# Performance work log

Measured on AMD Instinct MI355X. Metric: run time of the kernel, lower is better.

Reference implementation:

```python
import jax, jax.numpy as jnp
import numpy as np

DIM_Q = 1024
DIM_K = 1024
DIM_V = 1024


def setup_inputs() -> dict:
    key = jax.random.key(0)
    kx, kq, kk, kv = jax.random.split(key, 4)
    x = jax.random.normal(kx, (4, 2048, DIM_Q), dtype=jnp.float32)
    # torch nn.Linear weights: [out_features, in_features], y = x @ W.T
    scale = 1.0 / np.sqrt(DIM_Q)
    Wq = jax.random.uniform(kq, (DIM_K, DIM_Q), dtype=jnp.float32, minval=-scale, maxval=scale)
    Wk = jax.random.uniform(kk, (DIM_K, DIM_Q), dtype=jnp.float32, minval=-scale, maxval=scale)
    Wv = jax.random.uniform(kv, (DIM_V, DIM_Q), dtype=jnp.float32, minval=-scale, maxval=scale)
    return {"x": x, "Wq": Wq, "Wk": Wk, "Wv": Wv}


def reference(x, Wq, Wk, Wv):
    # q, k: [b, s, dim_k]; v: [b, s, dim_v]
    q = jnp.einsum('bsd,kd->bsk', x, Wq)
    k = jnp.einsum('bsd,kd->bsk', x, Wk)
    v = jnp.einsum('bsd,vd->bsv', x, Wv)
    norm_fact = 1.0 / jnp.sqrt(jnp.asarray(DIM_K, dtype=x.dtype))
    score = jnp.einsum('bik,bjk->bij', q, k) * norm_fact  # [b, s, s]
    score = jax.nn.softmax(score, axis=-1)
    att = jnp.einsum('bij,bjv->biv', score, v)
    att = att + v  # is_residual=True
    return att
```

## Files before the change

kernel.cpp:

```cpp
#include <hip/hip_runtime.h>
#include <hip/hip_bf16.h>

using bf16 = __hip_bfloat16;
typedef __attribute__((ext_vector_type(8))) short short8;
typedef __attribute__((ext_vector_type(4))) float floatx4;
typedef __attribute__((ext_vector_type(8))) int int8v;

__device__ __forceinline__ void async_ld16(const void* g, void* l) {
  __builtin_amdgcn_global_load_lds((const __attribute__((address_space(1))) void*)g,
                                   (__attribute__((address_space(3))) void*)l, 16, 0, 0);
}

__device__ __forceinline__ int pk4_fp8(float a, float b, float c, float d) {
  int v = __builtin_amdgcn_cvt_pk_fp8_f32(a, b, 0, false);
  return __builtin_amdgcn_cvt_pk_fp8_f32(c, d, v, true);
}

__device__ __forceinline__ int8v ld_frag16(const unsigned char* lo, const unsigned char* hi) {
  int4 l0 = *(const int4*)lo, h0 = *(const int4*)hi;
  int8v v;
  v[0] = l0.x; v[1] = l0.y; v[2] = l0.z; v[3] = l0.w;
  v[4] = h0.x; v[5] = h0.y; v[6] = h0.z; v[7] = h0.w;
  return v;
}


__device__ __forceinline__ void gemm_core(const bf16* __restrict__ At,
                                          const bf16* __restrict__ Bt,
                                          int K, bf16* lA, bf16* lB,
                                          floatx4 acc[4][4]) {
  const int tid  = threadIdx.x;
  const int w    = tid >> 6;
  const int lane = tid & 63;
  const int subM = (w >> 1) * 64;
  const int subN = (w & 1) * 64;
  const int fr   = lane & 15;
  const int fq   = lane >> 4;

  int srow[4], scol[4], sdst[4];
#pragma unroll
  for (int q = 0; q < 4; ++q) {
    int p = q * 256 + w * 64 + lane;
    int r = p >> 3;
    int j = (p & 7) ^ (r & 7);
    srow[q] = r;
    scol[q] = j * 8;
    sdst[q] = (q * 256 + w * 64) * 8;
  }
  int offA[2][4], offB[2][4];
#pragma unroll
  for (int kc = 0; kc < 2; ++kc)
#pragma unroll
    for (int i = 0; i < 4; ++i) {
      int rA = subM + i * 16 + fr;
      offA[kc][i] = (rA * 8 + ((kc * 4 + fq) ^ (rA & 7))) * 8;
      int rB = subN + i * 16 + fr;
      offB[kc][i] = (rB * 8 + ((kc * 4 + fq) ^ (rB & 7))) * 8;
    }

  floatx4 zero = {0.f, 0.f, 0.f, 0.f};
#pragma unroll
  for (int i = 0; i < 4; ++i)
#pragma unroll
    for (int j = 0; j < 4; ++j) acc[i][j] = zero;

  for (int k0 = 0; k0 < K; k0 += 64) {
    __syncthreads();
#pragma unroll
    for (int q = 0; q < 4; ++q) {
      async_ld16(At + (size_t)srow[q] * K + k0 + scol[q], lA + sdst[q]);
      async_ld16(Bt + (size_t)srow[q] * K + k0 + scol[q], lB + sdst[q]);
    }
    __syncthreads();
#pragma unroll
    for (int kc = 0; kc < 2; ++kc) {
      short8 a[4], b[4];
#pragma unroll
      for (int i = 0; i < 4; ++i) a[i] = *(const short8*)(lA + offA[kc][i]);
#pragma unroll
      for (int j = 0; j < 4; ++j) b[j] = *(const short8*)(lB + offB[kc][j]);
#pragma unroll
      for (int i = 0; i < 4; ++i)
#pragma unroll
        for (int j = 0; j < 4; ++j)
          acc[i][j] = __builtin_amdgcn_mfma_f32_16x16x32_bf16(a[i], b[j], acc[i][j], 0, 0, 0);
    }
  }
}

__device__ __forceinline__ void gemm_core_f8(const unsigned char* __restrict__ At,
                                             const unsigned char* __restrict__ Bt,
                                             int K, unsigned char* lA, unsigned char* lB,
                                             floatx4 acc[4][4]) {
  const int tid  = threadIdx.x;
  const int w    = tid >> 6;
  const int lane = tid & 63;
  const int subM = (w >> 1) * 64;
  const int subN = (w & 1) * 64;
  const int fr   = lane & 15;
  const int fq   = lane >> 4;

  int srow[4], scol[4], sdst[4];
#pragma unroll
  for (int q = 0; q < 4; ++q) {
    int p = q * 256 + w * 64 + lane;
    int r = p >> 3;
    int j = (p & 7) ^ (r & 7) ^ ((r & 8) >> 1);
    srow[q] = r;
    scol[q] = j * 16;
    sdst[q] = (q * 256 + w * 64) * 16;
  }
  int offA[2][4], offB[2][4];
#pragma unroll
  for (int h = 0; h < 2; ++h)
#pragma unroll
    for (int i = 0; i < 4; ++i) {
      int rA = subM + i * 16 + fr;
      offA[h][i] = rA * 128 + (((fq * 2 + h) ^ (rA & 7) ^ ((rA & 8) >> 1)) * 16);
      int rB = subN + i * 16 + fr;
      offB[h][i] = rB * 128 + (((fq * 2 + h) ^ (rB & 7) ^ ((rB & 8) >> 1)) * 16);
    }

  floatx4 zero = {0.f, 0.f, 0.f, 0.f};
#pragma unroll
  for (int i = 0; i < 4; ++i)
#pragma unroll
    for (int j = 0; j < 4; ++j) acc[i][j] = zero;

  for (int k0 = 0; k0 < K; k0 += 128) {
    __syncthreads();
#pragma unroll
    for (int q = 0; q < 4; ++q) {
      async_ld16(At + (size_t)srow[q] * K + k0 + scol[q], lA + sdst[q]);
      async_ld16(Bt + (size_t)srow[q] * K + k0 + scol[q], lB + sdst[q]);
    }
    __syncthreads();
    int8v a[4], b[4];
#pragma unroll
    for (int i = 0; i < 4; ++i) a[i] = ld_frag16(lA + offA[0][i], lA + offA[1][i]);
#pragma unroll
    for (int j = 0; j < 4; ++j) b[j] = ld_frag16(lB + offB[0][j], lB + offB[1][j]);
#pragma unroll
    for (int i = 0; i < 4; ++i)
#pragma unroll
      for (int j = 0; j < 4; ++j)
        acc[i][j] = __builtin_amdgcn_mfma_scale_f32_16x16x128_f8f6f4(
            a[i], b[j], acc[i][j], 0, 0, 0, 0x7F7F7F7F, 0, 0x7F7F7F7F);
  }
}

__device__ __forceinline__ void gemm_core_f8_v2(const unsigned char* __restrict__ At,
                                                const unsigned char* __restrict__ Bt,
                                                int K, unsigned char* lA, unsigned char* lB,
                                                floatx4 acc[4][8]) {
  const int tid  = threadIdx.x;
  const int w    = tid >> 6;
  const int lane = tid & 63;
  const int subM = (w >> 1) * 64;
  const int subN = (w & 1) * 128;
  const int fr   = lane & 15;
  const int fq   = lane >> 4;

  int srowA[4], scolA[4], sdstA[4];
#pragma unroll
  for (int q = 0; q < 4; ++q) {
    int p = q * 256 + w * 64 + lane;
    int r = p >> 3;
    int j = (p & 7) ^ (r & 7) ^ ((r & 8) >> 1);
    srowA[q] = r; scolA[q] = j * 16; sdstA[q] = (q * 256 + w * 64) * 16;
  }
  int srowB[8], scolB[8], sdstB[8];
#pragma unroll
  for (int q = 0; q < 8; ++q) {
    int p = q * 256 + w * 64 + lane;
    int r = p >> 3;
    int j = (p & 7) ^ (r & 7) ^ ((r & 8) >> 1);
    srowB[q] = r; scolB[q] = j * 16; sdstB[q] = (q * 256 + w * 64) * 16;
  }
  int offA[2][4], offB[2][8];
#pragma unroll
  for (int h = 0; h < 2; ++h) {
#pragma unroll
    for (int i = 0; i < 4; ++i) {
      int rA = subM + i * 16 + fr;
      offA[h][i] = rA * 128 + (((fq * 2 + h) ^ (rA & 7) ^ ((rA & 8) >> 1)) * 16);
    }
#pragma unroll
    for (int j = 0; j < 8; ++j) {
      int rB = subN + j * 16 + fr;
      offB[h][j] = rB * 128 + (((fq * 2 + h) ^ (rB & 7) ^ ((rB & 8) >> 1)) * 16);
    }
  }

  floatx4 zero = {0.f, 0.f, 0.f, 0.f};
#pragma unroll
  for (int i = 0; i < 4; ++i)
#pragma unroll
    for (int j = 0; j < 8; ++j) acc[i][j] = zero;

  for (int k0 = 0; k0 < K; k0 += 128) {
    __syncthreads();
#pragma unroll
    for (int q = 0; q < 4; ++q)
      async_ld16(At + (size_t)srowA[q] * K + k0 + scolA[q], lA + sdstA[q]);
#pragma unroll
    for (int q = 0; q < 8; ++q)
      async_ld16(Bt + (size_t)srowB[q] * K + k0 + scolB[q], lB + sdstB[q]);
    __syncthreads();
    int8v a[4];
#pragma unroll
    for (int i = 0; i < 4; ++i) a[i] = ld_frag16(lA + offA[0][i], lA + offA[1][i]);
#pragma unroll
    for (int j = 0; j < 8; ++j) {
      int8v bf = ld_frag16(lB + offB[0][j], lB + offB[1][j]);
#pragma unroll
      for (int i = 0; i < 4; ++i)
        acc[i][j] = __builtin_amdgcn_mfma_scale_f32_16x16x128_f8f6f4(
            a[i], bf, acc[i][j], 0, 0, 0, 0x7F7F7F7F, 0, 0x7F7F7F7F);
    }
  }
}

__global__ __launch_bounds__(256, 2) void proj_gemm(
    const bf16* __restrict__ Xbf, const bf16* __restrict__ Wvbf, bf16* __restrict__ Vbf,
    const unsigned char* __restrict__ X8, const unsigned char* __restrict__ Wq8,
    const unsigned char* __restrict__ Wk8,
    unsigned char* __restrict__ Qf8, unsigned char* __restrict__ Kf8) {
  __shared__ __align__(16) char lds[49152];
  const int id = blockIdx.x;
  const int tid = threadIdx.x, w = tid >> 6, lane = tid & 63;
  const int fr = lane & 15, fq = lane >> 4;

  if (id < 512) {
    const int r = id & 7, g = id >> 3;
    const int ty = r * 8 + (g & 7), tx = g >> 3;
    bf16* lA = (bf16*)lds;
    bf16* lB = (bf16*)(lds + 16384);
    floatx4 acc[4][4];
    gemm_core(Xbf + (size_t)ty * 128 * 1024, Wvbf + (size_t)tx * 128 * 1024,
              1024, lA, lB, acc);
    const int subM = (w >> 1) * 64, subN = (w & 1) * 64;
    const int rowBase = ty * 128 + subM;
    const int colBase = tx * 128 + subN;
#pragma unroll
    for (int i = 0; i < 4; ++i)
#pragma unroll
      for (int j = 0; j < 4; ++j)
#pragma unroll
        for (int rr = 0; rr < 4; ++rr) {
          int row = rowBase + i * 16 + fq * 4 + rr;
          int col = colBase + j * 16 + fr;
          Vbf[(size_t)row * 1024 + col] = __float2bfloat16(acc[i][j][rr]);
        }
  } else {
    const int local = id - 512;
    const int z = local >> 8, lid = local & 255;
    const int r = lid & 7, g = lid >> 3;
    const int ty = r * 8 + (g & 7);
    const int tx = g >> 3;
    unsigned char* lA = (unsigned char*)lds;
    unsigned char* lB = (unsigned char*)(lds + 16384);
    floatx4 acc[4][8];
    gemm_core_f8_v2(X8 + (size_t)ty * 128 * 1024,
                    (z == 0 ? Wq8 : Wk8) + (size_t)tx * 256 * 1024, 1024, lA, lB, acc);
    unsigned char* dst = (z == 0) ? Qf8 : Kf8;
    const int subM = (w >> 1) * 64, subN = (w & 1) * 128;
    const int rowBase = ty * 128 + subM;
    const int colBase = tx * 256 + subN;
#pragma unroll
    for (int i = 0; i < 4; ++i)
#pragma unroll
      for (int rr = 0; rr < 4; ++rr) {
        int row = rowBase + i * 16 + fq * 4 + rr;
        unsigned int p0 = (unsigned int)pk4_fp8(acc[i][0][rr], acc[i][1][rr],
                                                acc[i][2][rr], acc[i][3][rr]);
        unsigned int p1 = (unsigned int)pk4_fp8(acc[i][4][rr], acc[i][5][rr],
                                                acc[i][6][rr], acc[i][7][rr]);
        *(unsigned int*)&dst[(size_t)row * 1024 + colBase + fr * 4] = p0;
        *(unsigned int*)&dst[(size_t)row * 1024 + colBase + 64 + fr * 4] = p1;
      }
  }
}

__global__ __launch_bounds__(256, 2) void mid_kernel(
    const unsigned char* __restrict__ Qf8, const unsigned char* __restrict__ Kf8,
    unsigned char* __restrict__ S8, float* __restrict__ l,
    const bf16* __restrict__ Vbf, unsigned char* __restrict__ Vt8) {
  __shared__ __align__(16) char lds[49152];
  const int id = blockIdx.x;
  const int t = threadIdx.x;

  if (id < 512) {
    const int r = id & 7, g = id >> 3;
    const int b = g >> 4;
    const int rem = g & 15;
    const int ty = r * 2 + (rem & 1);
    const int tx = rem >> 1;
    unsigned char* lA = (unsigned char*)lds;
    unsigned char* lB = (unsigned char*)(lds + 16384);
    floatx4 acc[4][8];
    gemm_core_f8_v2(Qf8 + (size_t)b * 2048 * 1024 + (size_t)ty * 128 * 1024,
                    Kf8 + (size_t)b * 2048 * 1024 + (size_t)tx * 256 * 1024,
                    1024, lA, lB, acc);
    const int w = t >> 6, lane = t & 63;
    const int subM = (w >> 1) * 64, subN = (w & 1) * 128;
    const int fr = lane & 15, fq = lane >> 4;
    const int rowBase = ty * 128 + subM;
    const int colBase = tx * 256 + subN;
    unsigned char* Sb = S8 + (size_t)b * 2048 * 2048;
    float* lb = l + (size_t)b * 2048;
#pragma unroll
    for (int i = 0; i < 4; ++i)
#pragma unroll
      for (int rr = 0; rr < 4; ++rr) {
        int row = rowBase + i * 16 + fq * 4 + rr;
        unsigned int p0 = (unsigned int)pk4_fp8(
            __expf(acc[i][0][rr] * 0.03125f), __expf(acc[i][1][rr] * 0.03125f),
            __expf(acc[i][2][rr] * 0.03125f), __expf(acc[i][3][rr] * 0.03125f));
        unsigned int p1 = (unsigned int)pk4_fp8(
            __expf(acc[i][4][rr] * 0.03125f), __expf(acc[i][5][rr] * 0.03125f),
            __expf(acc[i][6][rr] * 0.03125f), __expf(acc[i][7][rr] * 0.03125f));
        *(unsigned int*)&Sb[(size_t)row * 2048 + colBase + fr * 4] = p0;
        *(unsigned int*)&Sb[(size_t)row * 2048 + colBase + 64 + fr * 4] = p1;
        float psum = __builtin_amdgcn_cvt_f32_fp8(p0, 0) + __builtin_amdgcn_cvt_f32_fp8(p0, 1) +
                     __builtin_amdgcn_cvt_f32_fp8(p0, 2) + __builtin_amdgcn_cvt_f32_fp8(p0, 3) +
                     __builtin_amdgcn_cvt_f32_fp8(p1, 0) + __builtin_amdgcn_cvt_f32_fp8(p1, 1) +
                     __builtin_amdgcn_cvt_f32_fp8(p1, 2) + __builtin_amdgcn_cvt_f32_fp8(p1, 3);
        psum += __shfl_xor(psum, 1, 64);
        psum += __shfl_xor(psum, 2, 64);
        psum += __shfl_xor(psum, 4, 64);
        psum += __shfl_xor(psum, 8, 64);
        if (fr == 0) atomicAdd(&lb[row], psum);
      }
  } else {
    const int t2 = id - 512;
    const int b = t2 >> 9, rem = t2 & 511;
    const int xs = rem & 31, yv = rem >> 5;
    const int s0 = xs * 64, v0 = yv * 64;
    short(*tile)[72] = (short(*)[72])lds;
#pragma unroll
    for (int i = 0; i < 2; ++i) {
      int c = t + i * 256;
      int row = c >> 3, cj = c & 7;
      *(short8*)&tile[row][cj * 8] =
          *(const short8*)&Vbf[((size_t)(b * 2048 + s0 + row)) * 1024 + v0 + cj * 8];
    }
    __syncthreads();
    const int vrow = t >> 2, sq = t & 3;
#pragma unroll
    for (int hc = 0; hc < 2; ++hc) {
      float f[8];
#pragma unroll
      for (int e = 0; e < 8; ++e) {
        int p = sq * 16 + hc * 8 + e;
        int s = (p & 3) * 16 + (p >> 2);
        short sh = tile[s][vrow];
        f[e] = __bfloat162float(*(bf16*)&sh);
      }
      uint2 packed;
      packed.x = (unsigned int)pk4_fp8(f[0], f[1], f[2], f[3]);
      packed.y = (unsigned int)pk4_fp8(f[4], f[5], f[6], f[7]);
      *(uint2*)&Vt8[((size_t)(b * 1024 + v0 + vrow)) * 2048 + s0 + sq * 16 + hc * 8] = packed;
    }
  }
}

__global__ __launch_bounds__(256) void pv_gemm(const unsigned char* __restrict__ S8,
                                               const unsigned char* __restrict__ Vt8,
                                               const bf16* __restrict__ Vbf,
                                               const float* __restrict__ l,
                                               float* __restrict__ out) {
  __shared__ __align__(16) char lds[32768];
  unsigned char* lA = (unsigned char*)lds;
  unsigned char* lB = (unsigned char*)(lds + 16384);
  const int id = blockIdx.x;
  const int r = id & 7, g = id >> 3;
  const int b = g >> 4;
  const int rem = g & 15;
  const int ty = r * 2 + (rem & 1);
  const int tx = rem >> 1;

  floatx4 acc[4][4];
  gemm_core_f8(S8 + (size_t)b * 2048 * 2048 + (size_t)ty * 128 * 2048,
               Vt8 + (size_t)b * 1024 * 2048 + (size_t)tx * 128 * 2048,
               2048, lA, lB, acc);

  const int tid = threadIdx.x, w = tid >> 6, lane = tid & 63;
  const int subM = (w >> 1) * 64, subN = (w & 1) * 64;
  const int fr = lane & 15, fq = lane >> 4;
  const int rowBase = ty * 128 + subM;
  const int colBase = tx * 128 + subN;
  const float* lb = l + (size_t)b * 2048;
#pragma unroll
  for (int i = 0; i < 4; ++i)
#pragma unroll
    for (int rr = 0; rr < 4; ++rr) {
      int row = rowBase + i * 16 + fq * 4 + rr;
      float inv = 1.0f / lb[row];
#pragma unroll
      for (int j = 0; j < 4; ++j) {
        int col = colBase + j * 16 + fr;
        size_t oi = ((size_t)b * 2048 + row) * 1024 + col;
        out[oi] = acc[i][j][rr] * inv + __bfloat162float(Vbf[oi]);
      }
    }
}

__global__ void cast_all(const float* __restrict__ x, const float* __restrict__ wq,
                         const float* __restrict__ wk, const float* __restrict__ wv,
                         bf16* __restrict__ Xbf, unsigned char* __restrict__ X8,
                         unsigned char* __restrict__ Wq8, unsigned char* __restrict__ Wk8,
                         bf16* __restrict__ Wvbf, float* __restrict__ l) {
  const int blk = blockIdx.x;
  const int t = threadIdx.x;
  if (blk < 2048) {
#pragma unroll
    for (int k = 0; k < 4; ++k) {
      int i = blk * 1024 + k * 256 + t;
      float4 f = ((const float4*)x)[i];
      bf16 tmp[4] = {__float2bfloat16(f.x), __float2bfloat16(f.y),
                     __float2bfloat16(f.z), __float2bfloat16(f.w)};
      ((ushort4*)Xbf)[i] = *(const ushort4*)tmp;
      ((unsigned int*)X8)[i] = (unsigned int)pk4_fp8(f.x, f.y, f.z, f.w);
    }
  } else if (blk < 2560) {
    const float* src = (blk < 2304) ? wq : wk;
    unsigned char* dst = (blk < 2304) ? Wq8 : Wk8;
    int base = ((blk - 2048) & 255) * 1024;
#pragma unroll
    for (int k = 0; k < 4; ++k) {
      int i = base + k * 256 + t;
      float4 f = ((const float4*)src)[i];
      ((unsigned int*)dst)[i] = (unsigned int)pk4_fp8(f.x, f.y, f.z, f.w);
    }
  } else if (blk < 2816) {
#pragma unroll
    for (int k = 0; k < 4; ++k) {
      int i = (blk - 2560) * 1024 + k * 256 + t;
      float4 f = ((const float4*)wv)[i];
      bf16 tmp[4] = {__float2bfloat16(f.x), __float2bfloat16(f.y),
                     __float2bfloat16(f.z), __float2bfloat16(f.w)};
      ((ushort4*)Wvbf)[i] = *(const ushort4*)tmp;
    }
  } else {
#pragma unroll
    for (int k = 0; k < 8; ++k)
      ((float4*)l)[k * 256 + t] = make_float4(0.f, 0.f, 0.f, 0.f);
  }
}

extern "C" void kernel_launch(void* const* d_in, const int* in_sizes, int n_in,
                              void* d_out, int out_size, void* d_ws, size_t ws_size,
                              hipStream_t stream) {
  const float* x  = (const float*)d_in[0];
  const float* Wq = (const float*)d_in[1];
  const float* Wk = (const float*)d_in[2];
  const float* Wv = (const float*)d_in[3];
  float* out = (float*)d_out;

  char* ws = (char*)d_ws;
  bf16* Xbf = (bf16*)ws;                   ws += (size_t)8192 * 1024 * 2;
  unsigned char* X8 = (unsigned char*)ws;  ws += (size_t)8192 * 1024;
  unsigned char* Wq8 = (unsigned char*)ws; ws += (size_t)1024 * 1024;
  unsigned char* Wk8 = (unsigned char*)ws; ws += (size_t)1024 * 1024;
  bf16* Wvbf = (bf16*)ws;                  ws += (size_t)1024 * 1024 * 2;
  unsigned char* Qf8 = (unsigned char*)ws; ws += (size_t)8192 * 1024;
  unsigned char* Kf8 = (unsigned char*)ws; ws += (size_t)8192 * 1024;
  bf16* Vbf = (bf16*)ws;                   ws += (size_t)8192 * 1024 * 2;
  unsigned char* Vt8 = (unsigned char*)ws; ws += (size_t)4 * 1024 * 2048;
  unsigned char* S8  = (unsigned char*)ws; ws += (size_t)4 * 2048 * 2048;
  float* l = (float*)ws;                   ws += (size_t)8192 * 4;

  cast_all<<<2817, 256, 0, stream>>>(x, Wq, Wk, Wv, Xbf, X8, Wq8, Wk8, Wvbf, l);
  proj_gemm<<<1024, 256, 0, stream>>>(Xbf, Wvbf, Vbf, X8, Wq8, Wk8, Qf8, Kf8);
  mid_kernel<<<2560, 256, 0, stream>>>(Qf8, Kf8, S8, l, Vbf, Vt8);
  pv_gemm<<<512, 256, 0, stream>>>(S8, Vt8, Vbf, l, out);
}
```

Before: 176.3 us.

## Double-buffer PV GEMM with 128x256 tiles and async prefetch pipeline

Rewrites the PV GEMM to use 128x256 output tiles, halving the grid to 256 blocks. It also adds a double-buffered LDS pipeline, so the next K-tile is prefetched with global_load_lds while MFMAs run on the current one, using explicit vmcnt waits and s_setprio. This is meant to hide global-load latency and raise reuse of each S tile, at the cost of 96KB LDS per block, which limits occupancy. With only 256 blocks on a 256-CU device, there is a single wave of work and little latency hiding across blocks. The final iteration issues a redundant prefetch of tile 0.

Measured after the change: 180.9 us. +2.6%, slower.

```diff
diff --git a/kernel.cpp b/kernel.cpp
--- a/kernel.cpp
+++ b/kernel.cpp
@@ -88,67 +88,6 @@
   }
 }
 
-__device__ __forceinline__ void gemm_core_f8(const unsigned char* __restrict__ At,
-                                             const unsigned char* __restrict__ Bt,
-                                             int K, unsigned char* lA, unsigned char* lB,
-                                             floatx4 acc[4][4]) {
-  const int tid  = threadIdx.x;
-  const int w    = tid >> 6;
-  const int lane = tid & 63;
-  const int subM = (w >> 1) * 64;
-  const int subN = (w & 1) * 64;
-  const int fr   = lane & 15;
-  const int fq   = lane >> 4;
-
-  int srow[4], scol[4], sdst[4];
-#pragma unroll
-  for (int q = 0; q < 4; ++q) {
-    int p = q * 256 + w * 64 + lane;
-    int r = p >> 3;
-    int j = (p & 7) ^ (r & 7) ^ ((r & 8) >> 1);
-    srow[q] = r;
-    scol[q] = j * 16;
-    sdst[q] = (q * 256 + w * 64) * 16;
-  }
-  int offA[2][4], offB[2][4];
-#pragma unroll
-  for (int h = 0; h < 2; ++h)
-#pragma unroll
-    for (int i = 0; i < 4; ++i) {
-      int rA = subM + i * 16 + fr;
-      offA[h][i] = rA * 128 + (((fq * 2 + h) ^ (rA & 7) ^ ((rA & 8) >> 1)) * 16);
-      int rB = subN + i * 16 + fr;
-      offB[h][i] = rB * 128 + (((fq * 2 + h) ^ (rB & 7) ^ ((rB & 8) >> 1)) * 16);
-    }
-
-  floatx4 zero = {0.f, 0.f, 0.f, 0.f};
-#pragma unroll
-  for (int i = 0; i < 4; ++i)
-#pragma unroll
-    for (int j = 0; j < 4; ++j) acc[i][j] = zero;
-
-  for (int k0 = 0; k0 < K; k0 += 128) {
-    __syncthreads();
-#pragma unroll
-    for (int q = 0; q < 4; ++q) {
-      async_ld16(At + (size_t)srow[q] * K + k0 + scol[q], lA + sdst[q]);
-      async_ld16(Bt + (size_t)srow[q] * K + k0 + scol[q], lB + sdst[q]);
-    }
-    __syncthreads();
-    int8v a[4], b[4];
-#pragma unroll
-    for (int i = 0; i < 4; ++i) a[i] = ld_frag16(lA + offA[0][i], lA + offA[1][i]);
-#pragma unroll
-    for (int j = 0; j < 4; ++j) b[j] = ld_frag16(lB + offB[0][j], lB + offB[1][j]);
-#pragma unroll
-    for (int i = 0; i < 4; ++i)
-#pragma unroll
-      for (int j = 0; j < 4; ++j)
-        acc[i][j] = __builtin_amdgcn_mfma_scale_f32_16x16x128_f8f6f4(
-            a[i], b[j], acc[i][j], 0, 0, 0, 0x7F7F7F7F, 0, 0x7F7F7F7F);
-  }
-}
-
 __device__ __forceinline__ void gemm_core_f8_v2(const unsigned char* __restrict__ At,
                                                 const unsigned char* __restrict__ Bt,
                                                 int K, unsigned char* lA, unsigned char* lB,
@@ -218,6 +157,97 @@
         acc[i][j] = __builtin_amdgcn_mfma_scale_f32_16x16x128_f8f6f4(
             a[i], bf, acc[i][j], 0, 0, 0, 0x7F7F7F7F, 0, 0x7F7F7F7F);
     }
+  }
+}
+
+__device__ __forceinline__ void gemm_core_f8_v2_dbuf(const unsigned char* __restrict__ At,
+                                                     const unsigned char* __restrict__ Bt,
+                                                     int K, unsigned char* lds0,
+                                                     floatx4 acc[4][8]) {
+  const int tid  = threadIdx.x;
+  const int w    = tid >> 6;
+  const int lane = tid & 63;
+  const int subM = (w >> 1) * 64;
+  const int subN = (w & 1) * 128;
+  const int fr   = lane & 15;
+  const int fq   = lane >> 4;
+
+  int srowA[4], scolA[4], sdstA[4];
+#pragma unroll
+  for (int q = 0; q < 4; ++q) {
+    int p = q * 256 + w * 64 + lane;
+    int r = p >> 3;
+    int j = (p & 7) ^ (r & 7) ^ ((r & 8) >> 1);
+    srowA[q] = r; scolA[q] = j * 16; sdstA[q] = (q * 256 + w * 64) * 16;
+  }
+  int srowB[8], scolB[8], sdstB[8];
+#pragma unroll
+  for (int q = 0; q < 8; ++q) {
+    int p = q * 256 + w * 64 + lane;
+    int r = p >> 3;
+    int j = (p & 7) ^ (r & 7) ^ ((r & 8) >> 1);
+    srowB[q] = r; scolB[q] = j * 16; sdstB[q] = (q * 256 + w * 64) * 16;
+  }
+  int offA[2][4], offB[2][8];
+#pragma unroll
+  for (int h = 0; h < 2; ++h) {
+#pragma unroll
+    for (int i = 0; i < 4; ++i) {
+      int rA = subM + i * 16 + fr;
+      offA[h][i] = rA * 128 + (((fq * 2 + h) ^ (rA & 7) ^ ((rA & 8) >> 1)) * 16);
+    }
+#pragma unroll
+    for (int j = 0; j < 8; ++j) {
+      int rB = subN + j * 16 + fr;
+      offB[h][j] = rB * 128 + (((fq * 2 + h) ^ (rB & 7) ^ ((rB & 8) >> 1)) * 16);
+    }
+  }
+
+  auto stage = [&](int buf, int k0) {
+    unsigned char* base = lds0 + buf * 49152;
+#pragma unroll
+    for (int q = 0; q < 4; ++q)
+      async_ld16(At + (size_t)srowA[q] * K + k0 + scolA[q], base + sdstA[q]);
+#pragma unroll
+    for (int q = 0; q < 8; ++q)
+      async_ld16(Bt + (size_t)srowB[q] * K + k0 + scolB[q], base + 16384 + sdstB[q]);
+  };
+
+  floatx4 zero = {0.f, 0.f, 0.f, 0.f};
+#pragma unroll
+  for (int i = 0; i < 4; ++i)
+#pragma unroll
+    for (int j = 0; j < 8; ++j) acc[i][j] = zero;
+
+  const int nt = K >> 7;
+  stage(0, 0);
+  asm volatile("s_waitcnt vmcnt(0)" ::: "memory");
+  __builtin_amdgcn_s_barrier();
+
+  for (int t = 0; t < nt; ++t) {
+    const int nb = (t + 1) & 1;
+    const int tn = (t + 1 < nt) ? (t + 1) : 0;
+    stage(nb, tn << 7);
+    asm volatile("s_waitcnt vmcnt(12)" ::: "memory");
+    __builtin_amdgcn_s_barrier();
+    __builtin_amdgcn_sched_barrier(0);
+
+    const unsigned char* lA = lds0 + (t & 1) * 49152;
+    const unsigned char* lB = lA + 16384;
+    int8v a[4];
+#pragma unroll
+    for (int i = 0; i < 4; ++i) a[i] = ld_frag16(lA + offA[0][i], lA + offA[1][i]);
+    __builtin_amdgcn_s_setprio(1);
+#pragma unroll
+    for (int j = 0; j < 8; ++j) {
+      int8v bf = ld_frag16(lB + offB[0][j], lB + offB[1][j]);
+#pragma unroll
+      for (int i = 0; i < 4; ++i)
+        acc[i][j] = __builtin_amdgcn_mfma_scale_f32_16x16x128_f8f6f4(
+            a[i], bf, acc[i][j], 0, 0, 0, 0x7F7F7F7F, 0, 0x7F7F7F7F);
+    }
+    __builtin_amdgcn_s_setprio(0);
+    __builtin_amdgcn_s_barrier();
   }
 }
 
@@ -370,26 +400,21 @@
                                                const bf16* __restrict__ Vbf,
                                                const float* __restrict__ l,
                                                float* __restrict__ out) {
-  __shared__ __align__(16) char lds[32768];
-  unsigned char* lA = (unsigned char*)lds;
-  unsigned char* lB = (unsigned char*)(lds + 16384);
+  __shared__ __align__(16) char lds[98304];
   const int id = blockIdx.x;
-  const int r = id & 7, g = id >> 3;
-  const int b = g >> 4;
-  const int rem = g & 15;
-  const int ty = r * 2 + (rem & 1);
-  const int tx = rem >> 1;
-
-  floatx4 acc[4][4];
-  gemm_core_f8(S8 + (size_t)b * 2048 * 2048 + (size_t)ty * 128 * 2048,
-               Vt8 + (size_t)b * 1024 * 2048 + (size_t)tx * 128 * 2048,
-               2048, lA, lB, acc);
+  const int pg = id & 15, ty = id >> 4;
+  const int b = pg >> 2, tx = pg & 3;
+
+  floatx4 acc[4][8];
+  gemm_core_f8_v2_dbuf(S8 + (size_t)b * 2048 * 2048 + (size_t)ty * 128 * 2048,
+                       Vt8 + (size_t)b * 1024 * 2048 + (size_t)tx * 256 * 2048,
+                       2048, (unsigned char*)lds, acc);
 
   const int tid = threadIdx.x, w = tid >> 6, lane = tid & 63;
-  const int subM = (w >> 1) * 64, subN = (w & 1) * 64;
+  const int subM = (w >> 1) * 64, subN = (w & 1) * 128;
   const int fr = lane & 15, fq = lane >> 4;
   const int rowBase = ty * 128 + subM;
-  const int colBase = tx * 128 + subN;
+  const int colBase = tx * 256 + subN;
   const float* lb = l + (size_t)b * 2048;
 #pragma unroll
   for (int i = 0; i < 4; ++i)
@@ -398,7 +423,7 @@
       int row = rowBase + i * 16 + fq * 4 + rr;
       float inv = 1.0f / lb[row];
 #pragma unroll
-      for (int j = 0; j < 4; ++j) {
+      for (int j = 0; j < 8; ++j) {
         int col = colBase + j * 16 + fr;
         size_t oi = ((size_t)b * 2048 + row) * 1024 + col;
         out[oi] = acc[i][j][rr] * inv + __bfloat162float(Vbf[oi]);
@@ -474,5 +499,5 @@
   cast_all<<<2817, 256, 0, stream>>>(x, Wq, Wk, Wv, Xbf, X8, Wq8, Wk8, Wvbf, l);
   proj_gemm<<<1024, 256, 0, stream>>>(Xbf, Wvbf, Vbf, X8, Wq8, Wk8, Qf8, Kf8);
   mid_kernel<<<2560, 256, 0, stream>>>(Qf8, Kf8, S8, l, Vbf, Vt8);
-  pv_gemm<<<512, 256, 0, stream>>>(S8, Vt8, Vbf, l, out);
-}
+  pv_gemm<<<256, 256, 0, stream>>>(S8, Vt8, Vbf, l, out);
+}
```
